# Kernel optimization log

Measured on AMD Instinct MI355X. Metric: run time of the kernel, lower is better.

The kernel has to match this reference:

```python
import jax, jax.numpy as jnp
import numpy as np

N, E, B = 200000, 1600000, 4096
IN_FEATS, H, R, NB = 64, 32, 8, 2


def _params(key):
    ks = jax.random.split(key, 20)
    p = {}
    dims = [(IN_FEATS, H), (H, H), (H, H), (H, H)]
    i = 0
    for l, (di, do) in enumerate(dims):
        p[f'basis{l}'] = jax.random.normal(ks[i], (NB, di, do), jnp.float32) * 0.1; i += 1
        p[f'comp{l}'] = jax.random.normal(ks[i], (R, NB), jnp.float32) * 0.1; i += 1
        p[f'wself{l}'] = jax.random.normal(ks[i], (di, do), jnp.float32) * 0.1; i += 1
        p[f'bias{l}'] = jnp.zeros((do,), jnp.float32); i += 1
    p['lin1_w'] = jax.random.normal(ks[i], (2 * 4 * H, 1), jnp.float32) * 0.05; i += 1
    p['lin1_b'] = jnp.zeros((1,), jnp.float32)
    return p


def setup_inputs() -> dict:
    key = jax.random.key(0)
    k = jax.random.split(key, 8)
    inp = {
        'x': jax.random.normal(k[0], (N, IN_FEATS), jnp.float32),
        'src': jax.random.randint(k[1], (E,), 0, N, jnp.int32),
        'dst': jax.random.randint(k[2], (E,), 0, N, jnp.int32),
        'etype': jax.random.randint(k[3], (E,), 0, R, jnp.int32),
        'user_idx': jax.random.randint(k[4], (B,), 0, N, jnp.int32),
        'item_idx': jax.random.randint(k[5], (B,), 0, N, jnp.int32),
    }
    inp.update(_params(k[6]))
    return inp


def _rel_graph_conv(x, src, dst, etype, basis, comp, wself, bias):
    # basis decomposition: W_r = sum_b comp[r,b] * basis[b]
    # compute per-node per-basis transform first (cheap: small NB), then mix per edge
    hb = jnp.einsum('ni,bio->nbo', x, basis)            # [N, NB, out]
    msg = jnp.einsum('eb,ebo->eo', comp[etype], hb[src])  # [E, out]
    agg = jax.ops.segment_sum(msg, dst, num_segments=x.shape[0])
    return agg + x @ wself + bias


def reference(x, src, dst, etype, user_idx, item_idx,
              basis0, comp0, wself0, bias0,
              basis1, comp1, wself1, bias1,
              basis2, comp2, wself2, bias2,
              basis3, comp3, wself3, bias3,
              lin1_w, lin1_b):
    states = []
    h = x
    for (ba, co, ws, bi) in ((basis0, comp0, wself0, bias0),
                             (basis1, comp1, wself1, bias1),
                             (basis2, comp2, wself2, bias2),
                             (basis3, comp3, wself3, bias3)):
        h = jnp.tanh(_rel_graph_conv(h, src, dst, etype, ba, co, ws, bi))
        states.append(h)
    cat = jnp.concatenate(states, axis=1)               # [N, 128]
    pair = jnp.concatenate([cat[user_idx], cat[item_idx]], axis=1)  # [B, 256]
    out = jax.nn.sigmoid(pair @ lin1_w + lin1_b)        # [B, 1]
    return out[:, 0]  # multiply_by == 1
```

## Files before the change

### kernel.cpp

```cpp
#include <hip/hip_runtime.h>
#include <hip/hip_bf16.h>


#define ETYPE_SHIFT 28
#define SRC_MASK 0x0FFFFFFFu
#define BUK_SH 9
#define BUK_W 512

typedef __attribute__((ext_vector_type(8))) short bf16x8;
typedef __attribute__((ext_vector_type(4))) float f32x4;

__device__ inline unsigned int f2bf(float f) {
    unsigned int u = __float_as_uint(f);
    return (u + 0x7FFFu + ((u >> 16) & 1u)) >> 16;
}

__device__ inline void block_exscan(int* a, int M, int* wsum ) {
    const int t = threadIdx.x;
    const int q = M >> 2;
    int s0 = 0, s1 = 0, s2 = 0, s3 = 0, s = 0;
    if (t < q) {
        s0 = a[4 * t]; s1 = a[4 * t + 1]; s2 = a[4 * t + 2]; s3 = a[4 * t + 3];
        s = s0 + s1 + s2 + s3;
    }
    int lane = t & 63, wid = t >> 6;
    int val = s;
    for (int d = 1; d < 64; d <<= 1) {
        int u = __shfl_up(val, d, 64);
        if (lane >= d) val += u;
    }
    if (lane == 63) wsum[wid] = val;
    __syncthreads();
    int woff = 0;
    for (int w = 0; w < wid; ++w) woff += wsum[w];
    val += woff;
    int base = val - s;
    __syncthreads();
    if (t < q) {
        a[4 * t]     = base;
        a[4 * t + 1] = base + s0;
        a[4 * t + 2] = base + s0 + s1;
        a[4 * t + 3] = base + s0 + s1 + s2;
    }
    __syncthreads();
}

__global__ __launch_bounds__(256) void k_buk_count(const int* __restrict__ dst,
                                                   int* __restrict__ gBukCnt, int E) {
    __shared__ int hist[1024];
    const int t = threadIdx.x;
    for (int f = t; f < 1024; f += 256) hist[f] = 0;
    __syncthreads();
    int e0 = blockIdx.x * 2048;
    for (int k = 0; k < 8; ++k) {
        int e = e0 + k * 256 + t;
        if (e < E) atomicAdd(&hist[dst[e] >> BUK_SH], 1);
    }
    __syncthreads();
    for (int f = t; f < 1024; f += 256) {
        int c = hist[f];
        if (c) atomicAdd(&gBukCnt[f], c);
    }
}

__global__ void k_buk_scan(const int* __restrict__ gBukCnt, int* __restrict__ bukOff,
                           int nb) {
    __shared__ int lds[1024];
    int tid = threadIdx.x;
    int v = (tid < nb) ? gBukCnt[tid] : 0;
    lds[tid] = v;
    __syncthreads();
    for (int d = 1; d < 1024; d <<= 1) {
        int u = (tid >= d) ? lds[tid - d] : 0;
        __syncthreads();
        lds[tid] += u;
        __syncthreads();
    }
    if (tid < nb) bukOff[tid] = lds[tid] - v;
    if (tid == nb - 1) bukOff[nb] = lds[tid];
}

__global__ __launch_bounds__(256) void k_binscatter(
    const int* __restrict__ src, const int* __restrict__ dst,
    const int* __restrict__ etype, const int* __restrict__ bukOff,
    int* __restrict__ gBukCur, unsigned long long* __restrict__ binned,
    int E, int NBUK)
{
    __shared__ int hist[1024];
    __shared__ int offs[1024];
    __shared__ int cur[1024];
    __shared__ int gb[1024];
    __shared__ int wsum[4];
    __shared__ unsigned long long stage[2048];
    const int t = threadIdx.x;
    for (int f = t; f < 1024; f += 256) { hist[f] = 0; cur[f] = 0; }
    __syncthreads();

    const int e0 = blockIdx.x * 2048;
    const int cntTot = min(2048, E - e0);
    unsigned long long pk[8];
    int bk[8];
#pragma unroll
    for (int k = 0; k < 8; ++k) {
        int e = e0 + k * 256 + t;
        if (e < E) {
            int d = dst[e];
            bk[k] = d >> BUK_SH;
            pk[k] = ((unsigned long long)(unsigned int)d << 32)
                  | (unsigned int)(src[e] | (etype[e] << ETYPE_SHIFT));
            atomicAdd(&hist[bk[k]], 1);
        } else bk[k] = -1;
    }
    __syncthreads();
    for (int f = t; f < 1024; f += 256) offs[f] = hist[f];
    __syncthreads();
    block_exscan(offs, 1024, wsum);
#pragma unroll
    for (int k = 0; k < 8; ++k) {
        if (bk[k] >= 0) {
            int pos = offs[bk[k]] + atomicAdd(&cur[bk[k]], 1);
            stage[pos] = pk[k];
        }
    }
    for (int f = t; f < NBUK; f += 256) {
        int c = hist[f];
        if (c > 0) gb[f] = bukOff[f] + atomicAdd(&gBukCur[f], c);
    }
    __syncthreads();
    for (int k = t; k < cntTot; k += 256) {
        unsigned long long v = stage[k];
        int b = (int)((unsigned int)(v >> 32) >> BUK_SH);
        binned[(size_t)gb[b] + (size_t)(k - offs[b])] = v;
    }
}

__global__ __launch_bounds__(256) void k_bucket_finalize(
    const unsigned long long* __restrict__ binned, const int* __restrict__ bukOff,
    int* __restrict__ rowptr, unsigned int* __restrict__ epack, int N, int E)
{
    __shared__ int nhist[512];
    __shared__ int ncur[512];
    __shared__ int wsum[4];
    const int t = threadIdx.x;
    const int b = blockIdx.x;
    for (int f = t; f < 512; f += 256) { nhist[f] = 0; ncur[f] = 0; }
    __syncthreads();
    const int k0 = bukOff[b], k1 = bukOff[b + 1];
    for (int k = k0 + t; k < k1; k += 256)
        atomicAdd(&nhist[(int)((unsigned int)(binned[k] >> 32) & (BUK_W - 1))], 1);
    __syncthreads();
    block_exscan(nhist, 512, wsum);
    for (int f = t; f < 512; f += 256) {
        int node = (b << BUK_SH) + f;
        if (node < N) rowptr[node] = k0 + nhist[f];
    }
    if (b == 0 && t == 0) rowptr[N] = E;
    for (int k = k0 + t; k < k1; k += 256) {
        unsigned long long v = binned[k];
        int dl = (int)((unsigned int)(v >> 32) & (BUK_W - 1));
        int pos = k0 + nhist[dl] + atomicAdd(&ncur[dl], 1);
        epack[pos] = (unsigned int)v;
    }
}

template<int DI>
__global__ __launch_bounds__(256) void k_transform3(
    const float* __restrict__ xin, int in_stride,
    const float* __restrict__ basis, const float* __restrict__ wself,
    const float* __restrict__ bias,
    unsigned int* __restrict__ hb2, float* __restrict__ selfout, int n)
{
    constexpr int ROWB = DI * 2;
    constexpr int SMASK = (ROWB / 16) - 1;
    constexpr int C4 = DI / 4;
    __shared__ unsigned short xs[64 * DI];
    __shared__ unsigned short bt[96 * DI];
    const int t = threadIdx.x;

    auto swz = [](int row, int byteInRow) -> int {
        int slot = (byteInRow >> 4) ^ ((row ^ (row >> 2)) & SMASK);
        return row * ROWB + (slot << 4) + (byteInRow & 15);
    };

    for (int f = t; f < 96 * C4; f += 256) {
        int k4 = f / 96;
        int o  = f - k4 * 96;
        const float* sp = (o < 64) ? (basis + (size_t)(o >> 5) * DI * 32 + (o & 31))
                                   : (wself + (o - 64));
        int k = 4 * k4;
        ushort4 pv;
        pv.x = (unsigned short)f2bf(sp[(size_t)(k + 0) * 32]);
        pv.y = (unsigned short)f2bf(sp[(size_t)(k + 1) * 32]);
        pv.z = (unsigned short)f2bf(sp[(size_t)(k + 2) * 32]);
        pv.w = (unsigned short)f2bf(sp[(size_t)(k + 3) * 32]);
        *(ushort4*)((char*)bt + swz(o, k * 2)) = pv;
    }

    const int node0 = blockIdx.x * 64;
    for (int f = t; f < 64 * C4; f += 256) {
        int nloc = f / C4, k4 = f - nloc * C4;
        int node = node0 + nloc;
        float4 v = make_float4(0.f, 0.f, 0.f, 0.f);
        if (node < n) v = *(const float4*)(xin + (size_t)node * in_stride + 4 * k4);
        ushort4 pv;
        pv.x = (unsigned short)f2bf(v.x);
        pv.y = (unsigned short)f2bf(v.y);
        pv.z = (unsigned short)f2bf(v.z);
        pv.w = (unsigned short)f2bf(v.w);
        *(ushort4*)((char*)xs + swz(nloc, 8 * k4)) = pv;
    }
    __syncthreads();

    const int w = t >> 6;
    const int l = t & 63;
    const int lr = l & 15;
    const int lg = l >> 4;

    f32x4 c[6];
#pragma unroll
    for (int i = 0; i < 6; ++i) c[i] = (f32x4){0.f, 0.f, 0.f, 0.f};

#pragma unroll
    for (int ks = 0; ks < DI / 32; ++ks) {
        const int kb = ks * 64 + lg * 16;
        bf16x8 a = *(const bf16x8*)((char*)xs + swz(w * 16 + lr, kb));
#pragma unroll
        for (int tt = 0; tt < 6; ++tt) {
            bf16x8 b = *(const bf16x8*)((char*)bt + swz(tt * 16 + lr, kb));
            c[tt] = __builtin_amdgcn_mfma_f32_16x16x32_bf16(a, b, c[tt], 0, 0, 0);
        }
    }

    const float bia0 = bias[lr];
    const float bia1 = bias[16 + lr];
#pragma unroll
    for (int r = 0; r < 4; ++r) {
        int node = node0 + w * 16 + lg * 4 + r;
        if (node < n) {
            hb2[(size_t)node * 32 + lr]      = f2bf(c[0][r]) | (f2bf(c[2][r]) << 16);
            hb2[(size_t)node * 32 + 16 + lr] = f2bf(c[1][r]) | (f2bf(c[3][r]) << 16);
            selfout[(size_t)node * 128 + lr]      = c[4][r] + bia0;
            selfout[(size_t)node * 128 + 16 + lr] = c[5][r] + bia1;
        }
    }
}

__global__ __launch_bounds__(256) void k_aggregate(
    const unsigned int* __restrict__ hb2,
    const unsigned int* __restrict__ epack,
    const int* __restrict__ rowptr,
    const float* __restrict__ comp,
    float* __restrict__ cat_l,
    int n)
{
    __shared__ unsigned int cw[8];
    if (threadIdx.x < 8)
        cw[threadIdx.x] = f2bf(comp[threadIdx.x * 2 + 0])
                        | (f2bf(comp[threadIdx.x * 2 + 1]) << 16);
    __syncthreads();
    int t = blockIdx.x * 256 + threadIdx.x;
    int node = t >> 4;
    int oj = t & 15;
    if (node >= n) return;
    float* cp = cat_l + (size_t)node * 128 + 2 * oj;
    float acc0 = cp[0];
    float acc1 = cp[1];
    const int k0 = rowptr[node], k1 = rowptr[node + 1];
    const unsigned gbase = (unsigned)oj * 8u;
    for (int k = k0; k < k1; k += 8) {
        unsigned int pp[8];
        uint2 hh[8];
#pragma unroll
        for (int j = 0; j < 8; ++j) {
            unsigned kk = (unsigned)min(k + j, k1 - 1);
            pp[j] = *(const unsigned int*)((const char*)epack + kk * 4u);
        }
#pragma unroll
        for (int j = 0; j < 8; ++j) {
            unsigned boff = (pp[j] & SRC_MASK) * 128u + gbase;
            hh[j] = *(const uint2*)((const char*)hb2 + boff);
        }
#pragma unroll
        for (int j = 0; j < 8; ++j) {
            bool valid = (k + j) < k1;
            unsigned w = cw[pp[j] >> ETYPE_SHIFT];
            unsigned hx = valid ? hh[j].x : 0u;
            unsigned hy = valid ? hh[j].y : 0u;
            float w0 = __uint_as_float(w << 16);
            float w1 = __uint_as_float(w & 0xFFFF0000u);
            acc0 = fmaf(w0, __uint_as_float(hx << 16), acc0);
            acc0 = fmaf(w1, __uint_as_float(hx & 0xFFFF0000u), acc0);
            acc1 = fmaf(w0, __uint_as_float(hy << 16), acc1);
            acc1 = fmaf(w1, __uint_as_float(hy & 0xFFFF0000u), acc1);
        }
    }
    float2 r;
    r.x = tanhf(acc0);
    r.y = tanhf(acc1);
    *(float2*)cp = r;
}

__global__ void k_head(const float* __restrict__ cat, const int* __restrict__ uidx,
                       const int* __restrict__ iidx, const float* __restrict__ w,
                       const float* __restrict__ b, float* __restrict__ out, int B) {
    int p = blockIdx.x;
    if (p >= B) return;
    int lane = threadIdx.x;
    const float* cu = cat + (size_t)uidx[p] * 128;
    const float* ci = cat + (size_t)iidx[p] * 128;
    float s = 0.f;
    s = fmaf(cu[lane], w[lane], s);
    s = fmaf(cu[lane + 64], w[lane + 64], s);
    s = fmaf(ci[lane], w[lane + 128], s);
    s = fmaf(ci[lane + 64], w[lane + 192], s);
    for (int d = 32; d > 0; d >>= 1) s += __shfl_down(s, d, 64);
    if (lane == 0) out[p] = 1.f / (1.f + expf(-(s + b[0])));
}

extern "C" void kernel_launch(void* const* d_in, const int* in_sizes, int n_in,
                              void* d_out, int out_size, void* d_ws, size_t ws_size,
                              hipStream_t stream) {
    const float* x      = (const float*)d_in[0];
    const int*   src    = (const int*)d_in[1];
    const int*   dst    = (const int*)d_in[2];
    const int*   etype  = (const int*)d_in[3];
    const int*   uidx   = (const int*)d_in[4];
    const int*   iidx   = (const int*)d_in[5];
    const float* lin1_w = (const float*)d_in[22];
    const float* lin1_b = (const float*)d_in[23];

    const int N = in_sizes[0] / 64;
    const int E = in_sizes[1];
    const int B = in_sizes[4];
    const int NBUK = (N + BUK_W - 1) >> BUK_SH;

    char* p = (char*)d_ws;
    auto alloc = [&](size_t bytes) -> void* {
        void* r = (void*)p;
        p += (bytes + 255) & ~(size_t)255;
        return r;
    };
    unsigned int*       hb2     = (unsigned int*)alloc((size_t)N * 32 * sizeof(unsigned int));
    float*              cat     = (float*)alloc((size_t)N * 128 * sizeof(float));
    int*                rowptr  = (int*)alloc((size_t)(N + 1) * sizeof(int));
    unsigned int*       epack   = (unsigned int*)alloc((size_t)E * sizeof(unsigned int));
    unsigned long long* binned  = (unsigned long long*)alloc((size_t)E * sizeof(unsigned long long));
    int*                gBukCnt = (int*)alloc(1024 * sizeof(int));
    int*                gBukCur = (int*)alloc(1024 * sizeof(int));
    int*                bukOff  = (int*)alloc(1025 * sizeof(int));

    hipMemsetAsync(gBukCnt, 0, 2048 * sizeof(int), stream);
    int ebGrid = (E + 2047) / 2048;
    k_buk_count<<<ebGrid, 256, 0, stream>>>(dst, gBukCnt, E);
    k_buk_scan<<<1, 1024, 0, stream>>>(gBukCnt, bukOff, NBUK);
    k_binscatter<<<ebGrid, 256, 0, stream>>>(src, dst, etype, bukOff, gBukCur,
                                             binned, E, NBUK);
    k_bucket_finalize<<<NBUK, 256, 0, stream>>>(binned, bukOff, rowptr, epack, N, E);

    int tr_grid = (N + 63) / 64;
    int agg_grid = (N * 16 + 255) / 256;
    for (int l = 0; l < 4; ++l) {
        const float* xin   = (l == 0) ? x : (cat + (size_t)(l - 1) * 32);
        int in_stride      = (l == 0) ? 64 : 128;
        const float* basis = (const float*)d_in[6 + l * 4];
        const float* comp  = (const float*)d_in[7 + l * 4];
        const float* wself = (const float*)d_in[8 + l * 4];
        const float* bias  = (const float*)d_in[9 + l * 4];
        if (l == 0)
            k_transform3<64><<<tr_grid, 256, 0, stream>>>(xin, in_stride, basis, wself,
                                                          bias, hb2, cat + (size_t)l * 32, N);
        else
            k_transform3<32><<<tr_grid, 256, 0, stream>>>(xin, in_stride, basis, wself,
                                                          bias, hb2, cat + (size_t)l * 32, N);
        k_aggregate<<<agg_grid, 256, 0, stream>>>(hb2, epack, rowptr, comp,
                                                  cat + (size_t)l * 32, N);
    }

    k_head<<<B, 64, 0, stream>>>(cat, uidx, iidx, lin1_w, lin1_b, (float*)d_out, B);
}
```

Measured before the change: 292.1 us.

## Pack binned edges into 32 bits and widen aggregation gathers to 16 bytes

Edge binning now packs src (18 bits), the local dst offset and etype into one 32-bit word. The bucket id is kept in a separate shared-memory array, which halves the global traffic of the binned intermediate. The aggregation kernel now uses 8 threads per node, each gathering a 16-byte hb2 chunk and accumulating four outputs, so there are fewer, wider loads and half as many epack/rowptr reads per node. tanhf is replaced with an exp/rcp approximation. The packing only holds if N fits in 18 bits, which matches the fixed N=200000 here.

```diff
diff --git a/kernel.cpp b/kernel.cpp
--- a/kernel.cpp
+++ b/kernel.cpp
@@ -2,8 +2,7 @@
 #include <hip/hip_bf16.h>
 
 
-#define ETYPE_SHIFT 28
-#define SRC_MASK 0x0FFFFFFFu
+#define SRC_MASK 0x3FFFFu
 #define BUK_SH 9
 #define BUK_W 512
 
@@ -13,6 +12,12 @@
 __device__ inline unsigned int f2bf(float f) {
     unsigned int u = __float_as_uint(f);
     return (u + 0x7FFFu + ((u >> 16) & 1u)) >> 16;
+}
+
+__device__ inline float fast_tanh(float x) {
+    float xc = fminf(fmaxf(x, -15.f), 15.f);
+    float e = __expf(2.f * xc);
+    return (e - 1.f) * __builtin_amdgcn_rcpf(e + 1.f);
 }
 
 __device__ inline void block_exscan(int* a, int M, int* wsum ) {
@@ -83,7 +88,7 @@
 __global__ __launch_bounds__(256) void k_binscatter(
     const int* __restrict__ src, const int* __restrict__ dst,
     const int* __restrict__ etype, const int* __restrict__ bukOff,
-    int* __restrict__ gBukCur, unsigned long long* __restrict__ binned,
+    int* __restrict__ gBukCur, unsigned int* __restrict__ binned,
     int E, int NBUK)
 {
     __shared__ int hist[1024];
@@ -91,14 +96,15 @@
     __shared__ int cur[1024];
     __shared__ int gb[1024];
     __shared__ int wsum[4];
-    __shared__ unsigned long long stage[2048];
+    __shared__ unsigned int stage[2048];
+    __shared__ unsigned short stageB[2048];
     const int t = threadIdx.x;
     for (int f = t; f < 1024; f += 256) { hist[f] = 0; cur[f] = 0; }
     __syncthreads();
 
     const int e0 = blockIdx.x * 2048;
     const int cntTot = min(2048, E - e0);
-    unsigned long long pk[8];
+    unsigned int pk[8];
     int bk[8];
 #pragma unroll
     for (int k = 0; k < 8; ++k) {
@@ -106,8 +112,9 @@
         if (e < E) {
             int d = dst[e];
             bk[k] = d >> BUK_SH;
-            pk[k] = ((unsigned long long)(unsigned int)d << 32)
-                  | (unsigned int)(src[e] | (etype[e] << ETYPE_SHIFT));
+            pk[k] = (unsigned int)src[e]
+                  | ((unsigned int)etype[e] << 29)
+                  | ((unsigned int)(d & (BUK_W - 1)) << 20);
             atomicAdd(&hist[bk[k]], 1);
         } else bk[k] = -1;
     }
@@ -120,6 +127,7 @@
         if (bk[k] >= 0) {
             int pos = offs[bk[k]] + atomicAdd(&cur[bk[k]], 1);
             stage[pos] = pk[k];
+            stageB[pos] = (unsigned short)bk[k];
         }
     }
     for (int f = t; f < NBUK; f += 256) {
@@ -128,14 +136,13 @@
     }
     __syncthreads();
     for (int k = t; k < cntTot; k += 256) {
-        unsigned long long v = stage[k];
-        int b = (int)((unsigned int)(v >> 32) >> BUK_SH);
-        binned[(size_t)gb[b] + (size_t)(k - offs[b])] = v;
+        int b = stageB[k];
+        binned[(size_t)gb[b] + (size_t)(k - offs[b])] = stage[k];
     }
 }
 
 __global__ __launch_bounds__(256) void k_bucket_finalize(
-    const unsigned long long* __restrict__ binned, const int* __restrict__ bukOff,
+    const unsigned int* __restrict__ binned, const int* __restrict__ bukOff,
     int* __restrict__ rowptr, unsigned int* __restrict__ epack, int N, int E)
 {
     __shared__ int nhist[512];
@@ -147,7 +154,7 @@
     __syncthreads();
     const int k0 = bukOff[b], k1 = bukOff[b + 1];
     for (int k = k0 + t; k < k1; k += 256)
-        atomicAdd(&nhist[(int)((unsigned int)(binned[k] >> 32) & (BUK_W - 1))], 1);
+        atomicAdd(&nhist[(binned[k] >> 20) & (BUK_W - 1)], 1);
     __syncthreads();
     block_exscan(nhist, 512, wsum);
     for (int f = t; f < 512; f += 256) {
@@ -156,10 +163,10 @@
     }
     if (b == 0 && t == 0) rowptr[N] = E;
     for (int k = k0 + t; k < k1; k += 256) {
-        unsigned long long v = binned[k];
-        int dl = (int)((unsigned int)(v >> 32) & (BUK_W - 1));
+        unsigned int v = binned[k];
+        int dl = (v >> 20) & (BUK_W - 1);
         int pos = k0 + nhist[dl] + atomicAdd(&ncur[dl], 1);
-        epack[pos] = (unsigned int)v;
+        epack[pos] = v & 0xE003FFFFu;
     }
 }
 
@@ -259,45 +266,50 @@
                         | (f2bf(comp[threadIdx.x * 2 + 1]) << 16);
     __syncthreads();
     int t = blockIdx.x * 256 + threadIdx.x;
-    int node = t >> 4;
-    int oj = t & 15;
+    int node = t >> 3;
+    int oj = t & 7;
     if (node >= n) return;
-    float* cp = cat_l + (size_t)node * 128 + 2 * oj;
-    float acc0 = cp[0];
-    float acc1 = cp[1];
+    float* cp = cat_l + (size_t)node * 128 + 4 * oj;
+    float4 acc = *(float4*)cp;
     const int k0 = rowptr[node], k1 = rowptr[node + 1];
-    const unsigned gbase = (unsigned)oj * 8u;
+    const unsigned gbase = (unsigned)oj * 16u;
     for (int k = k0; k < k1; k += 8) {
         unsigned int pp[8];
-        uint2 hh[8];
-#pragma unroll
-        for (int j = 0; j < 8; ++j) {
-            unsigned kk = (unsigned)min(k + j, k1 - 1);
-            pp[j] = *(const unsigned int*)((const char*)epack + kk * 4u);
-        }
+        uint4 hh[8];
+#pragma unroll
+        for (int j = 0; j < 8; ++j)
+            pp[j] = epack[min(k + j, k1 - 1)];
 #pragma unroll
         for (int j = 0; j < 8; ++j) {
             unsigned boff = (pp[j] & SRC_MASK) * 128u + gbase;
-            hh[j] = *(const uint2*)((const char*)hb2 + boff);
+            hh[j] = *(const uint4*)((const char*)hb2 + boff);
         }
 #pragma unroll
         for (int j = 0; j < 8; ++j) {
             bool valid = (k + j) < k1;
-            unsigned w = cw[pp[j] >> ETYPE_SHIFT];
+            unsigned w = cw[pp[j] >> 29];
+            float w0 = __uint_as_float(w << 16);
+            float w1 = __uint_as_float(w & 0xFFFF0000u);
             unsigned hx = valid ? hh[j].x : 0u;
             unsigned hy = valid ? hh[j].y : 0u;
-            float w0 = __uint_as_float(w << 16);
-            float w1 = __uint_as_float(w & 0xFFFF0000u);
-            acc0 = fmaf(w0, __uint_as_float(hx << 16), acc0);
-            acc0 = fmaf(w1, __uint_as_float(hx & 0xFFFF0000u), acc0);
-            acc1 = fmaf(w0, __uint_as_float(hy << 16), acc1);
-            acc1 = fmaf(w1, __uint_as_float(hy & 0xFFFF0000u), acc1);
-        }
-    }
-    float2 r;
-    r.x = tanhf(acc0);
-    r.y = tanhf(acc1);
-    *(float2*)cp = r;
+            unsigned hz = valid ? hh[j].z : 0u;
+            unsigned hw = valid ? hh[j].w : 0u;
+            acc.x = fmaf(w0, __uint_as_float(hx << 16), acc.x);
+            acc.x = fmaf(w1, __uint_as_float(hx & 0xFFFF0000u), acc.x);
+            acc.y = fmaf(w0, __uint_as_float(hy << 16), acc.y);
+            acc.y = fmaf(w1, __uint_as_float(hy & 0xFFFF0000u), acc.y);
+            acc.z = fmaf(w0, __uint_as_float(hz << 16), acc.z);
+            acc.z = fmaf(w1, __uint_as_float(hz & 0xFFFF0000u), acc.z);
+            acc.w = fmaf(w0, __uint_as_float(hw << 16), acc.w);
+            acc.w = fmaf(w1, __uint_as_float(hw & 0xFFFF0000u), acc.w);
+        }
+    }
+    float4 r;
+    r.x = fast_tanh(acc.x);
+    r.y = fast_tanh(acc.y);
+    r.z = fast_tanh(acc.z);
+    r.w = fast_tanh(acc.w);
+    *(float4*)cp = r;
 }
 
 __global__ void k_head(const float* __restrict__ cat, const int* __restrict__ uidx,
@@ -340,14 +352,14 @@
         p += (bytes + 255) & ~(size_t)255;
         return r;
     };
-    unsigned int*       hb2     = (unsigned int*)alloc((size_t)N * 32 * sizeof(unsigned int));
-    float*              cat     = (float*)alloc((size_t)N * 128 * sizeof(float));
-    int*                rowptr  = (int*)alloc((size_t)(N + 1) * sizeof(int));
-    unsigned int*       epack   = (unsigned int*)alloc((size_t)E * sizeof(unsigned int));
-    unsigned long long* binned  = (unsigned long long*)alloc((size_t)E * sizeof(unsigned long long));
-    int*                gBukCnt = (int*)alloc(1024 * sizeof(int));
-    int*                gBukCur = (int*)alloc(1024 * sizeof(int));
-    int*                bukOff  = (int*)alloc(1025 * sizeof(int));
+    unsigned int* hb2     = (unsigned int*)alloc((size_t)N * 32 * sizeof(unsigned int));
+    float*        cat     = (float*)alloc((size_t)N * 128 * sizeof(float));
+    int*          rowptr  = (int*)alloc((size_t)(N + 1) * sizeof(int));
+    unsigned int* epack   = (unsigned int*)alloc((size_t)E * sizeof(unsigned int));
+    unsigned int* binned  = (unsigned int*)alloc((size_t)E * sizeof(unsigned int));
+    int*          gBukCnt = (int*)alloc(1024 * sizeof(int));
+    int*          gBukCur = (int*)alloc(1024 * sizeof(int));
+    int*          bukOff  = (int*)alloc(1025 * sizeof(int));
 
     hipMemsetAsync(gBukCnt, 0, 2048 * sizeof(int), stream);
     int ebGrid = (E + 2047) / 2048;
@@ -358,7 +370,7 @@
     k_bucket_finalize<<<NBUK, 256, 0, stream>>>(binned, bukOff, rowptr, epack, N, E);
 
     int tr_grid = (N + 63) / 64;
-    int agg_grid = (N * 16 + 255) / 256;
+    int agg_grid = (N * 8 + 255) / 256;
     for (int l = 0; l < 4; ++l) {
         const float* xin   = (l == 0) ? x : (cat + (size_t)(l - 1) * 32);
         int in_stride      = (l == 0) ? 64 : 128;
```

New measurement: 291.6 us. No clear change (-0.2%).
